# Kernel optimization log

Hardware: AMD Instinct MI355X
Metric: run time of the kernel (lower is better)

## Reference

```python
import jax, jax.numpy as jnp
import numpy as np

N_NODES = 100000
N_EDGES = 3200000
N_GRAPHS = 1000
IN_C, HID_C, OUT_C = 128, 128, 10
BN_EPS = 1e-5


def setup_inputs() -> dict:
    key = jax.random.key(0)
    ks = jax.random.split(key, 16)
    s = lambda k, shape, fan: jax.random.normal(k, shape, jnp.float32) * (1.0 / np.sqrt(fan))
    x = jax.random.normal(ks[0], (N_NODES, IN_C), jnp.float32)
    edge_index = jax.random.randint(ks[1], (2, N_EDGES), 0, N_NODES, dtype=jnp.int64)
    batch = jnp.sort(jax.random.randint(ks[2], (N_NODES,), 0, N_GRAPHS, dtype=jnp.int64))
    return {
        "x": x, "edge_index": edge_index, "batch": batch,
        "W1a": s(ks[3], (IN_C, HID_C), IN_C), "b1a": jnp.zeros((HID_C,), jnp.float32),
        "W1b": s(ks[4], (HID_C, HID_C), HID_C), "b1b": jnp.zeros((HID_C,), jnp.float32),
        "g1": jnp.ones((HID_C,), jnp.float32), "be1": jnp.zeros((HID_C,), jnp.float32),
        "W2a": s(ks[5], (HID_C, HID_C), HID_C), "b2a": jnp.zeros((HID_C,), jnp.float32),
        "W2b": s(ks[6], (HID_C, HID_C), HID_C), "b2b": jnp.zeros((HID_C,), jnp.float32),
        "g2": jnp.ones((HID_C,), jnp.float32), "be2": jnp.zeros((HID_C,), jnp.float32),
        "Wlin": s(ks[7], (HID_C, OUT_C), HID_C), "blin": jnp.zeros((OUT_C,), jnp.float32),
    }


def _batchnorm(h, gamma, beta):
    # BatchNorm1d, training mode: batch statistics (biased variance, as torch)
    mean = jnp.mean(h, axis=0)
    var = jnp.mean(jnp.square(h - mean), axis=0)
    return (h - mean) * jax.lax.rsqrt(var + BN_EPS) * gamma + beta


def _gin_conv(x, src, dst, Wa, ba, Wb, bb, gamma, beta):
    # GINConv with eps=0: mlp(x + sum_{j->i} x_j); scatter-add over dst
    agg = jax.ops.segment_sum(x[src], dst, num_segments=N_NODES)
    h = x + agg
    h = jax.nn.relu(h @ Wa + ba) @ Wb + bb
    return _batchnorm(h, gamma, beta)


def reference(x, edge_index, batch, W1a, b1a, W1b, b1b, g1, be1,
              W2a, b2a, W2b, b2b, g2, be2, Wlin, blin):
    src, dst = edge_index[0], edge_index[1]
    h = jax.nn.relu(_gin_conv(x, src, dst, W1a, b1a, W1b, b1b, g1, be1))
    h = jax.nn.relu(_gin_conv(h, src, dst, W2a, b2a, W2b, b2b, g2, be2))
    pooled = jax.ops.segment_sum(h, batch, num_segments=N_GRAPHS)  # [G, HID_C]
    logits = pooled @ Wlin + blin
    return jax.nn.log_softmax(logits, axis=1)
```

## Files before the change

kernel.cpp:

```cpp
#include <hip/hip_runtime.h>
#include <hip/hip_bf16.h>

#define NN 100000
#define NE 3200000
#define NG 1000
#define BN_EPS 1e-5f

#define BKT_SH 6
#define BKTN 64
#define NBKT 1563
#define CHUNK 8192
#define NBINBLK 391

typedef __attribute__((ext_vector_type(8))) short short8v;
typedef __attribute__((ext_vector_type(4))) float f32x4;

__device__ __forceinline__ unsigned int f2bf(float f) {
    unsigned int u = __builtin_bit_cast(unsigned int, f);
    u += 0x7FFFu + ((u >> 16) & 1u);
    return u >> 16;
}
__device__ __forceinline__ float bf2f(unsigned int h16) {
    return __builtin_bit_cast(float, h16 << 16);
}

__global__ __launch_bounds__(256) void bucket_count_kernel(const int* __restrict__ dst,
                                                           int* __restrict__ bcnt) {
    __shared__ int h[NBKT];
    int t = threadIdx.x;
    for (int i = t; i < NBKT; i += 256) h[i] = 0;
    __syncthreads();
    int gid = blockIdx.x * 256 + t;
    for (int e = gid; e < NE; e += NBINBLK * 256) atomicAdd(&h[dst[e] >> BKT_SH], 1);
    __syncthreads();
    for (int i = t; i < NBKT; i += 256) if (h[i]) atomicAdd(&bcnt[i], h[i]);
}

__global__ void bucket_scan_kernel(const int* __restrict__ bcnt, int* __restrict__ bbase,
                                   int* __restrict__ bcur) {
    __shared__ int wsum[16];
    __shared__ int lcarry;
    int t = threadIdx.x, lane = t & 63, w = t >> 6;
    if (t == 0) lcarry = 0;
    __syncthreads();
    for (int base = 0; base < NBKT; base += 1024) {
        int i = base + t;
        int v = (i < NBKT) ? bcnt[i] : 0;
        int incl = v;
        #pragma unroll
        for (int d = 1; d < 64; d <<= 1) { int u = __shfl_up(incl, d, 64); if (lane >= d) incl += u; }
        if (lane == 63) wsum[w] = incl;
        __syncthreads();
        if (w == 0) {
            int s = (lane < 16) ? wsum[lane] : 0;
            #pragma unroll
            for (int d = 1; d < 16; d <<= 1) { int u = __shfl_up(s, d, 64); if (lane >= d) s += u; }
            if (lane < 16) wsum[lane] = s;
        }
        __syncthreads();
        int excl = lcarry + (w ? wsum[w - 1] : 0) + incl - v;
        if (i < NBKT) { bbase[i] = excl; bcur[i] = excl; }
        __syncthreads();
        if (t == 0) lcarry += wsum[15];
        __syncthreads();
    }
}

__global__ __launch_bounds__(256) void bin_kernel(const int* __restrict__ src,
        const int* __restrict__ dst, int* __restrict__ bcur,
        unsigned int* __restrict__ ebin) {
    __shared__ unsigned int ebuf[CHUNK];
    __shared__ unsigned short bids[CHUNK];
    __shared__ int hist[NBKT], lbase[NBKT], lcur[NBKT], delta[NBKT];
    __shared__ int wsum4[4];
    __shared__ int carry;
    int t = threadIdx.x;
    int lane = t & 63, w = t >> 6;
    int c0 = blockIdx.x * CHUNK;
    int cnt = min(CHUNK, NE - c0);
    for (int i = t; i < NBKT; i += 256) hist[i] = 0;
    if (t == 0) carry = 0;
    __syncthreads();
    for (int i = t; i < cnt; i += 256) atomicAdd(&hist[dst[c0 + i] >> BKT_SH], 1);
    __syncthreads();
    for (int bb = 0; bb < NBKT; bb += 256) {
        int i = bb + t;
        int v = (i < NBKT) ? hist[i] : 0;
        int incl = v;
        #pragma unroll
        for (int d2 = 1; d2 < 64; d2 <<= 1) { int u = __shfl_up(incl, d2, 64); if (lane >= d2) incl += u; }
        if (lane == 63) wsum4[w] = incl;
        __syncthreads();
        int wo = 0;
        if (w > 0) wo = wsum4[0];
        if (w > 1) wo += wsum4[1];
        if (w > 2) wo += wsum4[2];
        int excl = carry + wo + incl - v;
        if (i < NBKT) { lbase[i] = excl; lcur[i] = excl; }
        int tot = wsum4[0] + wsum4[1] + wsum4[2] + wsum4[3];
        __syncthreads();
        if (t == 0) carry += tot;
        __syncthreads();
    }
    for (int b = t; b < NBKT; b += 256) {
        int hh = hist[b];
        delta[b] = (hh ? atomicAdd(&bcur[b], hh) : 0) - lbase[b];
    }
    __syncthreads();
    for (int i = t; i < cnt; i += 256) {
        int d = dst[c0 + i];
        int s = src[c0 + i];
        int b = d >> BKT_SH;
        unsigned int entry = ((unsigned int)s << BKT_SH) | (unsigned int)(d & (BKTN - 1));
        int p = atomicAdd(&lcur[b], 1);
        ebuf[p] = entry;
        bids[p] = (unsigned short)b;
    }
    __syncthreads();
    for (int i = t; i < cnt; i += 256) {
        ebin[delta[bids[i]] + i] = ebuf[i];
    }
}

__global__ __launch_bounds__(256) void sort_kernel(const unsigned int* __restrict__ ebin,
        const int* __restrict__ bbase, const int* __restrict__ bcnt,
        int* __restrict__ noffs, int* __restrict__ csrc) {
    __shared__ int nh[BKTN], ncur[BKTN];
    int b = blockIdx.x, t = threadIdx.x;
    int base = bbase[b], cnt = bcnt[b];
    if (t < BKTN) nh[t] = 0;
    __syncthreads();
    for (int i = t; i < cnt; i += 256) atomicAdd(&nh[ebin[base + i] & (BKTN - 1)], 1);
    __syncthreads();
    if (t < 64) {
        int v = nh[t], incl = v;
        #pragma unroll
        for (int d = 1; d < 64; d <<= 1) { int u = __shfl_up(incl, d, 64); if (t >= d) incl += u; }
        int excl = incl - v;
        ncur[t] = excl;
        int node = (b << BKT_SH) + t;
        if (node < NN) noffs[node] = base + excl;
    }
    if (b == 0 && t == 0) noffs[NN] = NE;
    __syncthreads();
    for (int i = t; i < cnt; i += 256) {
        unsigned int e = ebin[base + i];
        int p = atomicAdd(&ncur[e & (BKTN - 1)], 1);
        csrc[base + p] = (int)(e >> BKT_SH);
    }
}

__global__ void prep_kernel(const float* __restrict__ x, unsigned int* __restrict__ xp,
                            const float* __restrict__ W1a, const float* __restrict__ W1b,
                            const float* __restrict__ W2a, const float* __restrict__ W2b,
                            unsigned int* __restrict__ Wt) {
    int bx = blockIdx.x;
    int t = threadIdx.x;
    if (bx < 25000) {
        int tid = bx * 256 + t;
        float2 v = ((const float2*)x)[tid];
        xp[tid] = f2bf(v.x) | (f2bf(v.y) << 16);
    } else {
        int tid = (bx - 25000) * 256 + t;
        int m = tid >> 13;
        int r = tid & 8191;
        int c = r >> 6, kh = r & 63;
        const float* W = (m == 0) ? W1a : (m == 1) ? W1b : (m == 2) ? W2a : W2b;
        float a = W[(2 * kh) * 128 + c];
        float b = W[(2 * kh + 1) * 128 + c];
        Wt[tid] = f2bf(a) | (f2bf(b) << 16);
    }
}

template<int BN_IN>
__global__ __launch_bounds__(256) void aggregate_gather_kernel(
        const unsigned int* __restrict__ xp, const float* __restrict__ coef,
        const int* __restrict__ noffs, const int* __restrict__ csrc,
        unsigned int* __restrict__ outp) {
    int node = __builtin_amdgcn_readfirstlane(blockIdx.x * 4 + (threadIdx.x >> 6));
    int lane = threadIdx.x & 63;
    float a0 = 1.f, b0 = 0.f, a1 = 1.f, b1 = 0.f;
    if (BN_IN) {
        float2 av = ((const float2*)coef)[lane];
        float2 bv = ((const float2*)(coef + 128))[lane];
        a0 = av.x; a1 = av.y; b0 = bv.x; b1 = bv.y;
    }
    unsigned int u = xp[(size_t)node * 64 + lane];
    float alo = bf2f(u & 0xFFFFu), ahi = bf2f(u >> 16);
    if (BN_IN) { alo = fmaxf(alo * a0 + b0, 0.f); ahi = fmaxf(ahi * a1 + b1, 0.f); }
    int s = noffs[node], e = noffs[node + 1];
    int i = s;
    for (; i + 16 <= e; i += 16) {
        int idx[16];
        #pragma unroll
        for (int j = 0; j < 16; ++j) idx[j] = csrc[i + j];
        unsigned int uv[16];
        #pragma unroll
        for (int j = 0; j < 16; ++j) uv[j] = xp[(size_t)idx[j] * 64 + lane];
        #pragma unroll
        for (int j = 0; j < 16; ++j) {
            float lo = bf2f(uv[j] & 0xFFFFu), hi = bf2f(uv[j] >> 16);
            if (BN_IN) { lo = fmaxf(lo * a0 + b0, 0.f); hi = fmaxf(hi * a1 + b1, 0.f); }
            alo += lo; ahi += hi;
        }
    }
    for (; i + 8 <= e; i += 8) {
        int idx[8];
        #pragma unroll
        for (int j = 0; j < 8; ++j) idx[j] = csrc[i + j];
        unsigned int uv[8];
        #pragma unroll
        for (int j = 0; j < 8; ++j) uv[j] = xp[(size_t)idx[j] * 64 + lane];
        #pragma unroll
        for (int j = 0; j < 8; ++j) {
            float lo = bf2f(uv[j] & 0xFFFFu), hi = bf2f(uv[j] >> 16);
            if (BN_IN) { lo = fmaxf(lo * a0 + b0, 0.f); hi = fmaxf(hi * a1 + b1, 0.f); }
            alo += lo; ahi += hi;
        }
    }
    for (; i < e; ++i) {
        int sv = csrc[i];
        unsigned int uu = xp[(size_t)sv * 64 + lane];
        float lo = bf2f(uu & 0xFFFFu), hi = bf2f(uu >> 16);
        if (BN_IN) { lo = fmaxf(lo * a0 + b0, 0.f); hi = fmaxf(hi * a1 + b1, 0.f); }
        alo += lo; ahi += hi;
    }
    outp[(size_t)node * 64 + lane] = f2bf(alo) | (f2bf(ahi) << 16);
}

__global__ __launch_bounds__(256) void mlp_kernel(const unsigned int* __restrict__ Pin,
        const unsigned int* __restrict__ WtA, const float* __restrict__ bA,
        const unsigned int* __restrict__ WtB, const float* __restrict__ bB,
        unsigned int* __restrict__ Pout, float* __restrict__ partial) {
    __shared__ unsigned int tile[64 * 68];
    __shared__ float sred[4][128];
    __shared__ float qred[4][128];
    int t = threadIdx.x, l = t & 63, w = t >> 6;
    int node0 = blockIdx.x * 64;
    int rbase = w * 16;
    int g = l >> 4, r = l & 15;
    int g4 = g * 4;

    const uint4* P4 = (const uint4*)Pin;
    #pragma unroll
    for (int i = 0; i < 4; ++i) {
        int rl = rbase + i * 4 + g;
        int node = node0 + rl;
        uint4 v = make_uint4(0u, 0u, 0u, 0u);
        if (node < NN) v = P4[(size_t)node * 16 + r];
        *(uint4*)&tile[rl * 68 + r * 4] = v;
    }

    f32x4 acc1[8];
    #pragma unroll
    for (int cb = 0; cb < 8; ++cb) acc1[cb] = (f32x4){0.f, 0.f, 0.f, 0.f};
    #pragma unroll
    for (int kk = 0; kk < 4; ++kk) {
        short8v a = *(short8v*)&tile[(rbase + r) * 68 + kk * 16 + g4];
        #pragma unroll
        for (int cb = 0; cb < 8; ++cb) {
            short8v wv = *(const short8v*)&WtA[(size_t)(cb * 16 + r) * 64 + kk * 16 + g4];
            acc1[cb] = __builtin_amdgcn_mfma_f32_16x16x32_bf16(wv, a, acc1[cb], 0, 0, 0);
        }
    }
    #pragma unroll
    for (int cb = 0; cb < 8; ++cb) {
        int c0 = cb * 16 + g4;
        float4 bi = *(const float4*)&bA[c0];
        float h0 = fmaxf(acc1[cb][0] + bi.x, 0.f);
        float h1 = fmaxf(acc1[cb][1] + bi.y, 0.f);
        float h2 = fmaxf(acc1[cb][2] + bi.z, 0.f);
        float h3 = fmaxf(acc1[cb][3] + bi.w, 0.f);
        uint2 pk;
        pk.x = f2bf(h0) | (f2bf(h1) << 16);
        pk.y = f2bf(h2) | (f2bf(h3) << 16);
        *(uint2*)&tile[(rbase + r) * 68 + (c0 >> 1)] = pk;
    }
    f32x4 acc2[8];
    #pragma unroll
    for (int cb = 0; cb < 8; ++cb) acc2[cb] = (f32x4){0.f, 0.f, 0.f, 0.f};
    #pragma unroll
    for (int kk = 0; kk < 4; ++kk) {
        short8v a = *(short8v*)&tile[(rbase + r) * 68 + kk * 16 + g4];
        #pragma unroll
        for (int cb = 0; cb < 8; ++cb) {
            short8v wv = *(const short8v*)&WtB[(size_t)(cb * 16 + r) * 64 + kk * 16 + g4];
            acc2[cb] = __builtin_amdgcn_mfma_f32_16x16x32_bf16(wv, a, acc2[cb], 0, 0, 0);
        }
    }
    int node = node0 + rbase + r;
    bool valid = node < NN;
    float msk = valid ? 1.f : 0.f;
    #pragma unroll
    for (int cb = 0; cb < 8; ++cb) {
        int c0 = cb * 16 + g4;
        float4 bi = *(const float4*)&bB[c0];
        float h0 = acc2[cb][0] + bi.x;
        float h1 = acc2[cb][1] + bi.y;
        float h2 = acc2[cb][2] + bi.z;
        float h3 = acc2[cb][3] + bi.w;
        float s0 = h0 * msk, s1 = h1 * msk, s2 = h2 * msk, s3 = h3 * msk;
        float q0 = s0 * h0, q1 = s1 * h1, q2 = s2 * h2, q3 = s3 * h3;
        #pragma unroll
        for (int m = 1; m < 16; m <<= 1) {
            s0 += __shfl_xor(s0, m, 64); s1 += __shfl_xor(s1, m, 64);
            s2 += __shfl_xor(s2, m, 64); s3 += __shfl_xor(s3, m, 64);
            q0 += __shfl_xor(q0, m, 64); q1 += __shfl_xor(q1, m, 64);
            q2 += __shfl_xor(q2, m, 64); q3 += __shfl_xor(q3, m, 64);
        }
        if (r == 0) {
            sred[w][c0 + 0] = s0; sred[w][c0 + 1] = s1;
            sred[w][c0 + 2] = s2; sred[w][c0 + 3] = s3;
            qred[w][c0 + 0] = q0; qred[w][c0 + 1] = q1;
            qred[w][c0 + 2] = q2; qred[w][c0 + 3] = q3;
        }
        if (valid) {
            uint2 pk;
            pk.x = f2bf(h0) | (f2bf(h1) << 16);
            pk.y = f2bf(h2) | (f2bf(h3) << 16);
            *(uint2*)&Pout[(size_t)node * 64 + (c0 >> 1)] = pk;
        }
    }
    __syncthreads();
    if (t < 128) {
        partial[(size_t)blockIdx.x * 256 + t] =
            sred[0][t] + sred[1][t] + sred[2][t] + sred[3][t];
    } else {
        int c = t - 128;
        partial[(size_t)blockIdx.x * 256 + t] =
            qred[0][c] + qred[1][c] + qred[2][c] + qred[3][c];
    }
}

__global__ __launch_bounds__(256) void bn_reduce_kernel(const float* __restrict__ partial,
        const float* __restrict__ gamma, const float* __restrict__ beta,
        float* __restrict__ coef) {
    __shared__ float red[2][256];
    int c = blockIdx.x;
    int t = threadIdx.x;
    float sm = 0.f, sq = 0.f;
    for (int i = t; i < NBKT; i += 256) {
        sm += partial[(size_t)i * 256 + c];
        sq += partial[(size_t)i * 256 + 128 + c];
    }
    red[0][t] = sm; red[1][t] = sq;
    __syncthreads();
    if (t < 64) {
        float s = red[0][t] + red[0][t + 64] + red[0][t + 128] + red[0][t + 192];
        float q = red[1][t] + red[1][t + 64] + red[1][t + 128] + red[1][t + 192];
        #pragma unroll
        for (int m = 1; m < 64; m <<= 1) {
            s += __shfl_xor(s, m, 64);
            q += __shfl_xor(q, m, 64);
        }
        if (t == 0) {
            const float inv = 1.0f / NN;
            float mean = s * inv;
            float var = q * inv - mean * mean;
            float a = gamma[c] * rsqrtf(var + BN_EPS);
            coef[c] = a;
            coef[128 + c] = beta[c] - mean * a;
        }
    }
}

__global__ void pool_head_kernel(const unsigned int* __restrict__ hb,
        const float* __restrict__ coef, const int* __restrict__ batch,
        const float* __restrict__ Wlin, const float* __restrict__ blin,
        float* __restrict__ out) {
    int g = blockIdx.x;
    int l = threadIdx.x;
    float2 av = ((const float2*)coef)[l];
    float2 bv = ((const float2*)(coef + 128))[l];
    int a = 0, b = NN;
    while (a < b) { int m = (a + b) >> 1; if (batch[m] < g) a = m + 1; else b = m; }
    int start = a;
    b = NN;
    while (a < b) { int m = (a + b) >> 1; if (batch[m] < g + 1) a = m + 1; else b = m; }
    int end = a;
    float s0 = 0.f, s1 = 0.f;
    for (int i = start; i < end; ++i) {
        unsigned int u = hb[(size_t)i * 64 + l];
        s0 += fmaxf(bf2f(u & 0xFFFFu) * av.x + bv.x, 0.f);
        s1 += fmaxf(bf2f(u >> 16) * av.y + bv.y, 0.f);
    }
    float lg[10];
    #pragma unroll
    for (int o = 0; o < 10; ++o) {
        float partial = s0 * Wlin[(2 * l) * 10 + o] + s1 * Wlin[(2 * l + 1) * 10 + o];
        #pragma unroll
        for (int m = 1; m < 64; m <<= 1) partial += __shfl_xor(partial, m, 64);
        lg[o] = partial + blin[o];
    }
    float mx = lg[0];
    #pragma unroll
    for (int o = 1; o < 10; ++o) mx = fmaxf(mx, lg[o]);
    float se = 0.f;
    #pragma unroll
    for (int o = 0; o < 10; ++o) se += expf(lg[o] - mx);
    float lse = mx + logf(se);
    if (l == 0) {
        #pragma unroll
        for (int o = 0; o < 10; ++o) out[g * 10 + o] = lg[o] - lse;
    }
}

extern "C" void kernel_launch(void* const* d_in, const int* in_sizes, int n_in,
                              void* d_out, int out_size, void* d_ws, size_t ws_size,
                              hipStream_t stream) {
    const float* x    = (const float*)d_in[0];
    const int*   edge = (const int*)d_in[1];
    const int*   batch= (const int*)d_in[2];
    const float* W1a  = (const float*)d_in[3];
    const float* b1a  = (const float*)d_in[4];
    const float* W1b  = (const float*)d_in[5];
    const float* b1b  = (const float*)d_in[6];
    const float* g1   = (const float*)d_in[7];
    const float* be1  = (const float*)d_in[8];
    const float* W2a  = (const float*)d_in[9];
    const float* b2a  = (const float*)d_in[10];
    const float* W2b  = (const float*)d_in[11];
    const float* b2b  = (const float*)d_in[12];
    const float* g2   = (const float*)d_in[13];
    const float* be2  = (const float*)d_in[14];
    const float* Wlin = (const float*)d_in[15];
    const float* blin = (const float*)d_in[16];
    float* out = (float*)d_out;

    char* ws = (char*)d_ws;
    size_t off = 0;
    auto alloc = [&](size_t bytes) -> void* {
        void* p = ws + off; off += (bytes + 255) & ~(size_t)255; return p;
    };
    unsigned int* Px   = (unsigned int*)alloc((size_t)NN * 64 * 4);
    unsigned int* Pa   = (unsigned int*)alloc((size_t)NN * 64 * 4);
    unsigned int* Pb   = (unsigned int*)alloc((size_t)NN * 64 * 4);
    unsigned int* ebin = (unsigned int*)alloc((size_t)NE * 4);
    int*   csrc   = (int*)alloc((size_t)NE * 4);
    int*   noffs  = (int*)alloc((NN + 1) * 4);
    int*   bcnt   = (int*)alloc(NBKT * 4);
    int*   bbase  = (int*)alloc(NBKT * 4);
    int*   bcur   = (int*)alloc(NBKT * 4);
    float* coef1  = (float*)alloc(256 * 4);
    float* coef2  = (float*)alloc(256 * 4);
    float* partial= (float*)alloc((size_t)NBKT * 256 * 4);
    unsigned int* Wt = (unsigned int*)alloc(4 * 8192 * 4);
    unsigned int* Wt1a = Wt;
    unsigned int* Wt1b = Wt + 8192;
    unsigned int* Wt2a = Wt + 16384;
    unsigned int* Wt2b = Wt + 24576;

    const int* srcI = edge;
    const int* dstI = edge + NE;

    hipMemsetAsync(bcnt, 0, NBKT * 4, stream);

    bucket_count_kernel<<<NBINBLK, 256, 0, stream>>>(dstI, bcnt);
    bucket_scan_kernel<<<1, 1024, 0, stream>>>(bcnt, bbase, bcur);
    bin_kernel<<<NBINBLK, 256, 0, stream>>>(srcI, dstI, bcur, ebin);
    sort_kernel<<<NBKT, 256, 0, stream>>>(ebin, bbase, bcnt, noffs, csrc);
    prep_kernel<<<25128, 256, 0, stream>>>(x, Px, W1a, W1b, W2a, W2b, Wt);

    aggregate_gather_kernel<0><<<25000, 256, 0, stream>>>(Px, coef1, noffs, csrc, Pa);
    mlp_kernel<<<NBKT, 256, 0, stream>>>(Pa, Wt1a, b1a, Wt1b, b1b, Pb, partial);
    bn_reduce_kernel<<<128, 256, 0, stream>>>(partial, g1, be1, coef1);
    aggregate_gather_kernel<1><<<25000, 256, 0, stream>>>(Pb, coef1, noffs, csrc, Pa);
    mlp_kernel<<<NBKT, 256, 0, stream>>>(Pa, Wt2a, b2a, Wt2b, b2b, Pb, partial);
    bn_reduce_kernel<<<128, 256, 0, stream>>>(partial, g2, be2, coef2);

    pool_head_kernel<<<NG, 64, 0, stream>>>(Pb, coef2, batch, Wlin, blin, out);
}
```

Measured before the change: 511.4 us.

## Sort CSR neighbors by source sub-range and fuse bucket count into prep

The per-bucket sort now keys on destination node plus a coarse source range (16 sub-ranges), so each node's neighbor list is ordered roughly by source index. This should improve locality of the feature gathers in both aggregation passes. Separately, the bucket-count pass is merged into the prep kernel as extra blocks, saving a launch and letting the two overlap. The cost is a larger shared histogram and a multi-pass block scan in the sort kernel.

Result: no change. 511.8 us (+0.1%).

```diff
diff --git a/kernel.cpp b/kernel.cpp
--- a/kernel.cpp
+++ b/kernel.cpp
@@ -11,6 +11,8 @@
 #define NBKT 1563
 #define CHUNK 8192
 #define NBINBLK 391
+#define NSR 16
+#define SRSH 13
 
 typedef __attribute__((ext_vector_type(8))) short short8v;
 typedef __attribute__((ext_vector_type(4))) float f32x4;
@@ -24,16 +26,36 @@
     return __builtin_bit_cast(float, h16 << 16);
 }
 
-__global__ __launch_bounds__(256) void bucket_count_kernel(const int* __restrict__ dst,
-                                                           int* __restrict__ bcnt) {
+__global__ void prep_kernel(const float* __restrict__ x, unsigned int* __restrict__ xp,
+                            const float* __restrict__ W1a, const float* __restrict__ W1b,
+                            const float* __restrict__ W2a, const float* __restrict__ W2b,
+                            unsigned int* __restrict__ Wt,
+                            const int* __restrict__ dst, int* __restrict__ bcnt) {
     __shared__ int h[NBKT];
+    int bx = blockIdx.x;
     int t = threadIdx.x;
-    for (int i = t; i < NBKT; i += 256) h[i] = 0;
-    __syncthreads();
-    int gid = blockIdx.x * 256 + t;
-    for (int e = gid; e < NE; e += NBINBLK * 256) atomicAdd(&h[dst[e] >> BKT_SH], 1);
-    __syncthreads();
-    for (int i = t; i < NBKT; i += 256) if (h[i]) atomicAdd(&bcnt[i], h[i]);
+    if (bx < 25000) {
+        int tid = bx * 256 + t;
+        float2 v = ((const float2*)x)[tid];
+        xp[tid] = f2bf(v.x) | (f2bf(v.y) << 16);
+    } else if (bx < 25128) {
+        int tid = (bx - 25000) * 256 + t;
+        int m = tid >> 13;
+        int r = tid & 8191;
+        int c = r >> 6, kh = r & 63;
+        const float* W = (m == 0) ? W1a : (m == 1) ? W1b : (m == 2) ? W2a : W2b;
+        float a = W[(2 * kh) * 128 + c];
+        float b = W[(2 * kh + 1) * 128 + c];
+        Wt[tid] = f2bf(a) | (f2bf(b) << 16);
+    } else {
+        int blk = bx - 25128;
+        for (int i = t; i < NBKT; i += 256) h[i] = 0;
+        __syncthreads();
+        int gid = blk * 256 + t;
+        for (int e = gid; e < NE; e += NBINBLK * 256) atomicAdd(&h[dst[e] >> BKT_SH], 1);
+        __syncthreads();
+        for (int i = t; i < NBKT; i += 256) if (h[i]) atomicAdd(&bcnt[i], h[i]);
+    }
 }
 
 __global__ void bucket_scan_kernel(const int* __restrict__ bcnt, int* __restrict__ bbase,
@@ -125,50 +147,51 @@
 __global__ __launch_bounds__(256) void sort_kernel(const unsigned int* __restrict__ ebin,
         const int* __restrict__ bbase, const int* __restrict__ bcnt,
         int* __restrict__ noffs, int* __restrict__ csrc) {
-    __shared__ int nh[BKTN], ncur[BKTN];
+    __shared__ int nh[BKTN * NSR];
+    __shared__ int wsum4[4];
+    __shared__ int carry;
     int b = blockIdx.x, t = threadIdx.x;
+    int lane = t & 63, w = t >> 6;
     int base = bbase[b], cnt = bcnt[b];
-    if (t < BKTN) nh[t] = 0;
-    __syncthreads();
-    for (int i = t; i < cnt; i += 256) atomicAdd(&nh[ebin[base + i] & (BKTN - 1)], 1);
-    __syncthreads();
-    if (t < 64) {
-        int v = nh[t], incl = v;
-        #pragma unroll
-        for (int d = 1; d < 64; d <<= 1) { int u = __shfl_up(incl, d, 64); if (t >= d) incl += u; }
-        int excl = incl - v;
-        ncur[t] = excl;
-        int node = (b << BKT_SH) + t;
-        if (node < NN) noffs[node] = base + excl;
-    }
-    if (b == 0 && t == 0) noffs[NN] = NE;
+    for (int i = t; i < BKTN * NSR; i += 256) nh[i] = 0;
+    if (t == 0) carry = 0;
     __syncthreads();
     for (int i = t; i < cnt; i += 256) {
         unsigned int e = ebin[base + i];
-        int p = atomicAdd(&ncur[e & (BKTN - 1)], 1);
-        csrc[base + p] = (int)(e >> BKT_SH);
-    }
-}
-
-__global__ void prep_kernel(const float* __restrict__ x, unsigned int* __restrict__ xp,
-                            const float* __restrict__ W1a, const float* __restrict__ W1b,
-                            const float* __restrict__ W2a, const float* __restrict__ W2b,
-                            unsigned int* __restrict__ Wt) {
-    int bx = blockIdx.x;
-    int t = threadIdx.x;
-    if (bx < 25000) {
-        int tid = bx * 256 + t;
-        float2 v = ((const float2*)x)[tid];
-        xp[tid] = f2bf(v.x) | (f2bf(v.y) << 16);
-    } else {
-        int tid = (bx - 25000) * 256 + t;
-        int m = tid >> 13;
-        int r = tid & 8191;
-        int c = r >> 6, kh = r & 63;
-        const float* W = (m == 0) ? W1a : (m == 1) ? W1b : (m == 2) ? W2a : W2b;
-        float a = W[(2 * kh) * 128 + c];
-        float b = W[(2 * kh + 1) * 128 + c];
-        Wt[tid] = f2bf(a) | (f2bf(b) << 16);
+        int key = (int)(e & (BKTN - 1)) * NSR + (int)((e >> BKT_SH) >> SRSH);
+        atomicAdd(&nh[key], 1);
+    }
+    __syncthreads();
+    for (int rb = 0; rb < BKTN * NSR; rb += 256) {
+        int v = nh[rb + t];
+        int incl = v;
+        #pragma unroll
+        for (int d = 1; d < 64; d <<= 1) { int u = __shfl_up(incl, d, 64); if (lane >= d) incl += u; }
+        if (lane == 63) wsum4[w] = incl;
+        __syncthreads();
+        int wo = 0;
+        if (w > 0) wo = wsum4[0];
+        if (w > 1) wo += wsum4[1];
+        if (w > 2) wo += wsum4[2];
+        int tot = wsum4[0] + wsum4[1] + wsum4[2] + wsum4[3];
+        int excl = carry + wo + incl - v;
+        nh[rb + t] = excl;
+        __syncthreads();
+        if (t == 0) carry += tot;
+        __syncthreads();
+    }
+    if (t < 64) {
+        int node = (b << BKT_SH) + t;
+        if (node < NN) noffs[node] = base + nh[t * NSR];
+    }
+    if (b == 0 && t == 0) noffs[NN] = NE;
+    __syncthreads();
+    for (int i = t; i < cnt; i += 256) {
+        unsigned int e = ebin[base + i];
+        int srcv = (int)(e >> BKT_SH);
+        int key = (int)(e & (BKTN - 1)) * NSR + (srcv >> SRSH);
+        int p = atomicAdd(&nh[key], 1);
+        csrc[base + p] = srcv;
     }
 }
 
@@ -455,11 +478,11 @@
 
     hipMemsetAsync(bcnt, 0, NBKT * 4, stream);
 
-    bucket_count_kernel<<<NBINBLK, 256, 0, stream>>>(dstI, bcnt);
+    prep_kernel<<<25128 + NBINBLK, 256, 0, stream>>>(x, Px, W1a, W1b, W2a, W2b, Wt,
+                                                     dstI, bcnt);
     bucket_scan_kernel<<<1, 1024, 0, stream>>>(bcnt, bbase, bcur);
     bin_kernel<<<NBINBLK, 256, 0, stream>>>(srcI, dstI, bcur, ebin);
     sort_kernel<<<NBKT, 256, 0, stream>>>(ebin, bbase, bcnt, noffs, csrc);
-    prep_kernel<<<25128, 256, 0, stream>>>(x, Px, W1a, W1b, W2a, W2b, Wt);
 
     aggregate_gather_kernel<0><<<25000, 256, 0, stream>>>(Px, coef1, noffs, csrc, Pa);
     mlp_kernel<<<NBKT, 256, 0, stream>>>(Pa, Wt1a, b1a, Wt1b, b1b, Pb, partial);
```

## Fuse bucket count into prep kernel and simplify binning with direct global scatter

Applied to the files above, without the earlier changes.

The bucket-count pass becomes extra blocks of the prep kernel, so counting overlaps with bf16 conversion and one launch disappears. The bin kernel drops its in-block prefix scan and shared staging buffer and writes each edge straight to its global slot via a shared per-bucket cursor. Chunk size shrinks so more blocks run with less shared memory. The trade-off is less coalesced global writes in binning and more global atomics on the bucket cursors.

Result: slower. 580.0 us (+13.4%).

```diff
diff --git a/kernel.cpp b/kernel.cpp
--- a/kernel.cpp
+++ b/kernel.cpp
@@ -9,8 +9,8 @@
 #define BKT_SH 6
 #define BKTN 64
 #define NBKT 1563
-#define CHUNK 8192
-#define NBINBLK 391
+#define CHUNK 2048
+#define NBINBLK 1563
 
 typedef __attribute__((ext_vector_type(8))) short short8v;
 typedef __attribute__((ext_vector_type(4))) float f32x4;
@@ -24,143 +24,19 @@
     return __builtin_bit_cast(float, h16 << 16);
 }
 
-__global__ __launch_bounds__(256) void bucket_count_kernel(const int* __restrict__ dst,
-                                                           int* __restrict__ bcnt) {
-    __shared__ int h[NBKT];
-    int t = threadIdx.x;
-    for (int i = t; i < NBKT; i += 256) h[i] = 0;
-    __syncthreads();
-    int gid = blockIdx.x * 256 + t;
-    for (int e = gid; e < NE; e += NBINBLK * 256) atomicAdd(&h[dst[e] >> BKT_SH], 1);
-    __syncthreads();
-    for (int i = t; i < NBKT; i += 256) if (h[i]) atomicAdd(&bcnt[i], h[i]);
-}
-
-__global__ void bucket_scan_kernel(const int* __restrict__ bcnt, int* __restrict__ bbase,
-                                   int* __restrict__ bcur) {
-    __shared__ int wsum[16];
-    __shared__ int lcarry;
-    int t = threadIdx.x, lane = t & 63, w = t >> 6;
-    if (t == 0) lcarry = 0;
-    __syncthreads();
-    for (int base = 0; base < NBKT; base += 1024) {
-        int i = base + t;
-        int v = (i < NBKT) ? bcnt[i] : 0;
-        int incl = v;
-        #pragma unroll
-        for (int d = 1; d < 64; d <<= 1) { int u = __shfl_up(incl, d, 64); if (lane >= d) incl += u; }
-        if (lane == 63) wsum[w] = incl;
-        __syncthreads();
-        if (w == 0) {
-            int s = (lane < 16) ? wsum[lane] : 0;
-            #pragma unroll
-            for (int d = 1; d < 16; d <<= 1) { int u = __shfl_up(s, d, 64); if (lane >= d) s += u; }
-            if (lane < 16) wsum[lane] = s;
-        }
-        __syncthreads();
-        int excl = lcarry + (w ? wsum[w - 1] : 0) + incl - v;
-        if (i < NBKT) { bbase[i] = excl; bcur[i] = excl; }
-        __syncthreads();
-        if (t == 0) lcarry += wsum[15];
-        __syncthreads();
-    }
-}
-
-__global__ __launch_bounds__(256) void bin_kernel(const int* __restrict__ src,
-        const int* __restrict__ dst, int* __restrict__ bcur,
-        unsigned int* __restrict__ ebin) {
-    __shared__ unsigned int ebuf[CHUNK];
-    __shared__ unsigned short bids[CHUNK];
-    __shared__ int hist[NBKT], lbase[NBKT], lcur[NBKT], delta[NBKT];
-    __shared__ int wsum4[4];
-    __shared__ int carry;
-    int t = threadIdx.x;
-    int lane = t & 63, w = t >> 6;
-    int c0 = blockIdx.x * CHUNK;
-    int cnt = min(CHUNK, NE - c0);
-    for (int i = t; i < NBKT; i += 256) hist[i] = 0;
-    if (t == 0) carry = 0;
-    __syncthreads();
-    for (int i = t; i < cnt; i += 256) atomicAdd(&hist[dst[c0 + i] >> BKT_SH], 1);
-    __syncthreads();
-    for (int bb = 0; bb < NBKT; bb += 256) {
-        int i = bb + t;
-        int v = (i < NBKT) ? hist[i] : 0;
-        int incl = v;
-        #pragma unroll
-        for (int d2 = 1; d2 < 64; d2 <<= 1) { int u = __shfl_up(incl, d2, 64); if (lane >= d2) incl += u; }
-        if (lane == 63) wsum4[w] = incl;
-        __syncthreads();
-        int wo = 0;
-        if (w > 0) wo = wsum4[0];
-        if (w > 1) wo += wsum4[1];
-        if (w > 2) wo += wsum4[2];
-        int excl = carry + wo + incl - v;
-        if (i < NBKT) { lbase[i] = excl; lcur[i] = excl; }
-        int tot = wsum4[0] + wsum4[1] + wsum4[2] + wsum4[3];
-        __syncthreads();
-        if (t == 0) carry += tot;
-        __syncthreads();
-    }
-    for (int b = t; b < NBKT; b += 256) {
-        int hh = hist[b];
-        delta[b] = (hh ? atomicAdd(&bcur[b], hh) : 0) - lbase[b];
-    }
-    __syncthreads();
-    for (int i = t; i < cnt; i += 256) {
-        int d = dst[c0 + i];
-        int s = src[c0 + i];
-        int b = d >> BKT_SH;
-        unsigned int entry = ((unsigned int)s << BKT_SH) | (unsigned int)(d & (BKTN - 1));
-        int p = atomicAdd(&lcur[b], 1);
-        ebuf[p] = entry;
-        bids[p] = (unsigned short)b;
-    }
-    __syncthreads();
-    for (int i = t; i < cnt; i += 256) {
-        ebin[delta[bids[i]] + i] = ebuf[i];
-    }
-}
-
-__global__ __launch_bounds__(256) void sort_kernel(const unsigned int* __restrict__ ebin,
-        const int* __restrict__ bbase, const int* __restrict__ bcnt,
-        int* __restrict__ noffs, int* __restrict__ csrc) {
-    __shared__ int nh[BKTN], ncur[BKTN];
-    int b = blockIdx.x, t = threadIdx.x;
-    int base = bbase[b], cnt = bcnt[b];
-    if (t < BKTN) nh[t] = 0;
-    __syncthreads();
-    for (int i = t; i < cnt; i += 256) atomicAdd(&nh[ebin[base + i] & (BKTN - 1)], 1);
-    __syncthreads();
-    if (t < 64) {
-        int v = nh[t], incl = v;
-        #pragma unroll
-        for (int d = 1; d < 64; d <<= 1) { int u = __shfl_up(incl, d, 64); if (t >= d) incl += u; }
-        int excl = incl - v;
-        ncur[t] = excl;
-        int node = (b << BKT_SH) + t;
-        if (node < NN) noffs[node] = base + excl;
-    }
-    if (b == 0 && t == 0) noffs[NN] = NE;
-    __syncthreads();
-    for (int i = t; i < cnt; i += 256) {
-        unsigned int e = ebin[base + i];
-        int p = atomicAdd(&ncur[e & (BKTN - 1)], 1);
-        csrc[base + p] = (int)(e >> BKT_SH);
-    }
-}
-
 __global__ void prep_kernel(const float* __restrict__ x, unsigned int* __restrict__ xp,
                             const float* __restrict__ W1a, const float* __restrict__ W1b,
                             const float* __restrict__ W2a, const float* __restrict__ W2b,
-                            unsigned int* __restrict__ Wt) {
+                            unsigned int* __restrict__ Wt,
+                            const int* __restrict__ dst, int* __restrict__ bcnt) {
+    __shared__ int h[NBKT];
     int bx = blockIdx.x;
     int t = threadIdx.x;
     if (bx < 25000) {
         int tid = bx * 256 + t;
         float2 v = ((const float2*)x)[tid];
         xp[tid] = f2bf(v.x) | (f2bf(v.y) << 16);
-    } else {
+    } else if (bx < 25128) {
         int tid = (bx - 25000) * 256 + t;
         int m = tid >> 13;
         int r = tid & 8191;
@@ -169,6 +45,100 @@
         float a = W[(2 * kh) * 128 + c];
         float b = W[(2 * kh + 1) * 128 + c];
         Wt[tid] = f2bf(a) | (f2bf(b) << 16);
+    } else {
+        int blk = bx - 25128;
+        for (int i = t; i < NBKT; i += 256) h[i] = 0;
+        __syncthreads();
+        int c0 = blk * CHUNK;
+        int cnt = min(CHUNK, NE - c0);
+        for (int i = t; i < cnt; i += 256) atomicAdd(&h[dst[c0 + i] >> BKT_SH], 1);
+        __syncthreads();
+        for (int i = t; i < NBKT; i += 256) if (h[i]) atomicAdd(&bcnt[i], h[i]);
+    }
+}
+
+__global__ void bucket_scan_kernel(const int* __restrict__ bcnt, int* __restrict__ bbase,
+                                   int* __restrict__ bcur) {
+    __shared__ int wsum[16];
+    __shared__ int lcarry;
+    int t = threadIdx.x, lane = t & 63, w = t >> 6;
+    if (t == 0) lcarry = 0;
+    __syncthreads();
+    for (int base = 0; base < NBKT; base += 1024) {
+        int i = base + t;
+        int v = (i < NBKT) ? bcnt[i] : 0;
+        int incl = v;
+        #pragma unroll
+        for (int d = 1; d < 64; d <<= 1) { int u = __shfl_up(incl, d, 64); if (lane >= d) incl += u; }
+        if (lane == 63) wsum[w] = incl;
+        __syncthreads();
+        if (w == 0) {
+            int s = (lane < 16) ? wsum[lane] : 0;
+            #pragma unroll
+            for (int d = 1; d < 16; d <<= 1) { int u = __shfl_up(s, d, 64); if (lane >= d) s += u; }
+            if (lane < 16) wsum[lane] = s;
+        }
+        __syncthreads();
+        int excl = lcarry + (w ? wsum[w - 1] : 0) + incl - v;
+        if (i < NBKT) { bbase[i] = excl; bcur[i] = excl; }
+        __syncthreads();
+        if (t == 0) lcarry += wsum[15];
+        __syncthreads();
+    }
+}
+
+__global__ __launch_bounds__(256) void bin_kernel(const int* __restrict__ src,
+        const int* __restrict__ dst, int* __restrict__ bcur,
+        unsigned int* __restrict__ ebin) {
+    __shared__ int hist[NBKT];
+    __shared__ int delta[NBKT];
+    __shared__ int lcur[NBKT];
+    int t = threadIdx.x;
+    int c0 = blockIdx.x * CHUNK;
+    int cnt = min(CHUNK, NE - c0);
+    for (int i = t; i < NBKT; i += 256) { hist[i] = 0; lcur[i] = 0; }
+    __syncthreads();
+    for (int i = t; i < cnt; i += 256) atomicAdd(&hist[dst[c0 + i] >> BKT_SH], 1);
+    __syncthreads();
+    for (int b = t; b < NBKT; b += 256) {
+        int hh = hist[b];
+        delta[b] = hh ? atomicAdd(&bcur[b], hh) : 0;
+    }
+    __syncthreads();
+    for (int i = t; i < cnt; i += 256) {
+        int d = dst[c0 + i];
+        int s = src[c0 + i];
+        int b = d >> BKT_SH;
+        int p = atomicAdd(&lcur[b], 1);
+        ebin[delta[b] + p] = ((unsigned int)s << BKT_SH) | (unsigned int)(d & (BKTN - 1));
+    }
+}
+
+__global__ __launch_bounds__(256) void sort_kernel(const unsigned int* __restrict__ ebin,
+        const int* __restrict__ bbase, const int* __restrict__ bcnt,
+        int* __restrict__ noffs, int* __restrict__ csrc) {
+    __shared__ int nh[BKTN], ncur[BKTN];
+    int b = blockIdx.x, t = threadIdx.x;
+    int base = bbase[b], cnt = bcnt[b];
+    if (t < BKTN) nh[t] = 0;
+    __syncthreads();
+    for (int i = t; i < cnt; i += 256) atomicAdd(&nh[ebin[base + i] & (BKTN - 1)], 1);
+    __syncthreads();
+    if (t < 64) {
+        int v = nh[t], incl = v;
+        #pragma unroll
+        for (int d = 1; d < 64; d <<= 1) { int u = __shfl_up(incl, d, 64); if (t >= d) incl += u; }
+        int excl = incl - v;
+        ncur[t] = excl;
+        int node = (b << BKT_SH) + t;
+        if (node < NN) noffs[node] = base + excl;
+    }
+    if (b == 0 && t == 0) noffs[NN] = NE;
+    __syncthreads();
+    for (int i = t; i < cnt; i += 256) {
+        unsigned int e = ebin[base + i];
+        int p = atomicAdd(&ncur[e & (BKTN - 1)], 1);
+        csrc[base + p] = (int)(e >> BKT_SH);
     }
 }
 
@@ -455,11 +425,11 @@
 
     hipMemsetAsync(bcnt, 0, NBKT * 4, stream);
 
-    bucket_count_kernel<<<NBINBLK, 256, 0, stream>>>(dstI, bcnt);
+    prep_kernel<<<25128 + NBINBLK, 256, 0, stream>>>(x, Px, W1a, W1b, W2a, W2b, Wt,
+                                                     dstI, bcnt);
     bucket_scan_kernel<<<1, 1024, 0, stream>>>(bcnt, bbase, bcur);
     bin_kernel<<<NBINBLK, 256, 0, stream>>>(srcI, dstI, bcur, ebin);
     sort_kernel<<<NBKT, 256, 0, stream>>>(ebin, bbase, bcnt, noffs, csrc);
-    prep_kernel<<<25128, 256, 0, stream>>>(x, Px, W1a, W1b, W2a, W2b, Wt);
 
     aggregate_gather_kernel<0><<<25000, 256, 0, stream>>>(Px, coef1, noffs, csrc, Pa);
     mlp_kernel<<<NBKT, 256, 0, stream>>>(Pa, Wt1a, b1a, Wt1b, b1b, Pb, partial);
```

## Widen CSR buckets to 128 nodes and fuse bucket counting into prep kernel

Applied to the files above, without the earlier changes.

Doubles the destination bucket width to 128 nodes, which halves the bucket count to 782, and halves the bin chunk size so the binning stage still launches 782 blocks. The bucket-count histogram is folded into the bf16 conversion prep kernel as extra blocks, removing one launch. The scan becomes a single pass because the bucket count now fits in one block, and the sort kernel scans 128 per-node counts with two wavefront scans. The MLP tile count is decoupled into a separate NTILE constant so the MLP grid is unchanged. In exchange, each sort block handles larger buckets and the bin kernel works on smaller chunks with more scatter runs.

New measurement: 534.5 us. 4.5% more time.

```diff
diff --git a/kernel.cpp b/kernel.cpp
--- a/kernel.cpp
+++ b/kernel.cpp
@@ -6,11 +6,14 @@
 #define NG 1000
 #define BN_EPS 1e-5f
 
-#define BKT_SH 6
-#define BKTN 64
-#define NBKT 1563
-#define CHUNK 8192
-#define NBINBLK 391
+#define BKT_SH 7
+#define BKTN 128
+#define NBKT 782
+#define CHUNK 4096
+#define NBINBLK 782
+#define HCHUNK 2048
+#define NHBLK 1563
+#define NTILE 1563
 
 typedef __attribute__((ext_vector_type(8))) short short8v;
 typedef __attribute__((ext_vector_type(4))) float f32x4;
@@ -24,46 +27,58 @@
     return __builtin_bit_cast(float, h16 << 16);
 }
 
-__global__ __launch_bounds__(256) void bucket_count_kernel(const int* __restrict__ dst,
-                                                           int* __restrict__ bcnt) {
+__global__ void prep_kernel(const float* __restrict__ x, unsigned int* __restrict__ xp,
+                            const float* __restrict__ W1a, const float* __restrict__ W1b,
+                            const float* __restrict__ W2a, const float* __restrict__ W2b,
+                            unsigned int* __restrict__ Wt,
+                            const int* __restrict__ dst, int* __restrict__ bcnt) {
     __shared__ int h[NBKT];
+    int bx = blockIdx.x;
     int t = threadIdx.x;
-    for (int i = t; i < NBKT; i += 256) h[i] = 0;
-    __syncthreads();
-    int gid = blockIdx.x * 256 + t;
-    for (int e = gid; e < NE; e += NBINBLK * 256) atomicAdd(&h[dst[e] >> BKT_SH], 1);
-    __syncthreads();
-    for (int i = t; i < NBKT; i += 256) if (h[i]) atomicAdd(&bcnt[i], h[i]);
+    if (bx < 25000) {
+        int tid = bx * 256 + t;
+        float2 v = ((const float2*)x)[tid];
+        xp[tid] = f2bf(v.x) | (f2bf(v.y) << 16);
+    } else if (bx < 25128) {
+        int tid = (bx - 25000) * 256 + t;
+        int m = tid >> 13;
+        int r = tid & 8191;
+        int c = r >> 6, kh = r & 63;
+        const float* W = (m == 0) ? W1a : (m == 1) ? W1b : (m == 2) ? W2a : W2b;
+        float a = W[(2 * kh) * 128 + c];
+        float b = W[(2 * kh + 1) * 128 + c];
+        Wt[tid] = f2bf(a) | (f2bf(b) << 16);
+    } else {
+        int blk = bx - 25128;
+        for (int i = t; i < NBKT; i += 256) h[i] = 0;
+        __syncthreads();
+        int c0 = blk * HCHUNK;
+        int cnt = min(HCHUNK, NE - c0);
+        for (int i = t; i < cnt; i += 256) atomicAdd(&h[dst[c0 + i] >> BKT_SH], 1);
+        __syncthreads();
+        for (int i = t; i < NBKT; i += 256) if (h[i]) atomicAdd(&bcnt[i], h[i]);
+    }
 }
 
 __global__ void bucket_scan_kernel(const int* __restrict__ bcnt, int* __restrict__ bbase,
                                    int* __restrict__ bcur) {
     __shared__ int wsum[16];
-    __shared__ int lcarry;
     int t = threadIdx.x, lane = t & 63, w = t >> 6;
-    if (t == 0) lcarry = 0;
-    __syncthreads();
-    for (int base = 0; base < NBKT; base += 1024) {
-        int i = base + t;
-        int v = (i < NBKT) ? bcnt[i] : 0;
-        int incl = v;
-        #pragma unroll
-        for (int d = 1; d < 64; d <<= 1) { int u = __shfl_up(incl, d, 64); if (lane >= d) incl += u; }
-        if (lane == 63) wsum[w] = incl;
-        __syncthreads();
-        if (w == 0) {
-            int s = (lane < 16) ? wsum[lane] : 0;
-            #pragma unroll
-            for (int d = 1; d < 16; d <<= 1) { int u = __shfl_up(s, d, 64); if (lane >= d) s += u; }
-            if (lane < 16) wsum[lane] = s;
-        }
-        __syncthreads();
-        int excl = lcarry + (w ? wsum[w - 1] : 0) + incl - v;
-        if (i < NBKT) { bbase[i] = excl; bcur[i] = excl; }
-        __syncthreads();
-        if (t == 0) lcarry += wsum[15];
-        __syncthreads();
-    }
+    int v = (t < NBKT) ? bcnt[t] : 0;
+    int incl = v;
+    #pragma unroll
+    for (int d = 1; d < 64; d <<= 1) { int u = __shfl_up(incl, d, 64); if (lane >= d) incl += u; }
+    if (lane == 63) wsum[w] = incl;
+    __syncthreads();
+    if (w == 0) {
+        int s = (lane < 16) ? wsum[lane] : 0;
+        #pragma unroll
+        for (int d = 1; d < 16; d <<= 1) { int u = __shfl_up(s, d, 64); if (lane >= d) s += u; }
+        if (lane < 16) wsum[lane] = s;
+    }
+    __syncthreads();
+    int excl = (w ? wsum[w - 1] : 0) + incl - v;
+    if (t < NBKT) { bbase[t] = excl; bcur[t] = excl; }
 }
 
 __global__ __launch_bounds__(256) void bin_kernel(const int* __restrict__ src,
@@ -125,7 +140,7 @@
 __global__ __launch_bounds__(256) void sort_kernel(const unsigned int* __restrict__ ebin,
         const int* __restrict__ bbase, const int* __restrict__ bcnt,
         int* __restrict__ noffs, int* __restrict__ csrc) {
-    __shared__ int nh[BKTN], ncur[BKTN];
+    __shared__ int nh[BKTN], nbase[BKTN], ncur[BKTN];
     int b = blockIdx.x, t = threadIdx.x;
     int base = bbase[b], cnt = bcnt[b];
     if (t < BKTN) nh[t] = 0;
@@ -133,13 +148,22 @@
     for (int i = t; i < cnt; i += 256) atomicAdd(&nh[ebin[base + i] & (BKTN - 1)], 1);
     __syncthreads();
     if (t < 64) {
-        int v = nh[t], incl = v;
-        #pragma unroll
-        for (int d = 1; d < 64; d <<= 1) { int u = __shfl_up(incl, d, 64); if (t >= d) incl += u; }
-        int excl = incl - v;
-        ncur[t] = excl;
-        int node = (b << BKT_SH) + t;
-        if (node < NN) noffs[node] = base + excl;
+        int v0 = nh[t], v1 = nh[64 + t];
+        int i0 = v0;
+        #pragma unroll
+        for (int d = 1; d < 64; d <<= 1) { int u = __shfl_up(i0, d, 64); if (t >= d) i0 += u; }
+        int tot0 = __shfl(i0, 63, 64);
+        int i1 = v1;
+        #pragma unroll
+        for (int d = 1; d < 64; d <<= 1) { int u = __shfl_up(i1, d, 64); if (t >= d) i1 += u; }
+        int e0 = i0 - v0;
+        int e1 = tot0 + i1 - v1;
+        nbase[t] = e0; nbase[64 + t] = e1;
+        ncur[t] = e0; ncur[64 + t] = e1;
+        int node0 = (b << BKT_SH) + t;
+        int node1 = node0 + 64;
+        if (node0 < NN) noffs[node0] = base + e0;
+        if (node1 < NN) noffs[node1] = base + e1;
     }
     if (b == 0 && t == 0) noffs[NN] = NE;
     __syncthreads();
@@ -147,28 +171,6 @@
         unsigned int e = ebin[base + i];
         int p = atomicAdd(&ncur[e & (BKTN - 1)], 1);
         csrc[base + p] = (int)(e >> BKT_SH);
-    }
-}
-
-__global__ void prep_kernel(const float* __restrict__ x, unsigned int* __restrict__ xp,
-                            const float* __restrict__ W1a, const float* __restrict__ W1b,
-                            const float* __restrict__ W2a, const float* __restrict__ W2b,
-                            unsigned int* __restrict__ Wt) {
-    int bx = blockIdx.x;
-    int t = threadIdx.x;
-    if (bx < 25000) {
-        int tid = bx * 256 + t;
-        float2 v = ((const float2*)x)[tid];
-        xp[tid] = f2bf(v.x) | (f2bf(v.y) << 16);
-    } else {
-        int tid = (bx - 25000) * 256 + t;
-        int m = tid >> 13;
-        int r = tid & 8191;
-        int c = r >> 6, kh = r & 63;
-        const float* W = (m == 0) ? W1a : (m == 1) ? W1b : (m == 2) ? W2a : W2b;
-        float a = W[(2 * kh) * 128 + c];
-        float b = W[(2 * kh + 1) * 128 + c];
-        Wt[tid] = f2bf(a) | (f2bf(b) << 16);
     }
 }
 
@@ -339,7 +341,7 @@
     int c = blockIdx.x;
     int t = threadIdx.x;
     float sm = 0.f, sq = 0.f;
-    for (int i = t; i < NBKT; i += 256) {
+    for (int i = t; i < NTILE; i += 256) {
         sm += partial[(size_t)i * 256 + c];
         sq += partial[(size_t)i * 256 + 128 + c];
     }
@@ -443,7 +445,7 @@
     int*   bcur   = (int*)alloc(NBKT * 4);
     float* coef1  = (float*)alloc(256 * 4);
     float* coef2  = (float*)alloc(256 * 4);
-    float* partial= (float*)alloc((size_t)NBKT * 256 * 4);
+    float* partial= (float*)alloc((size_t)NTILE * 256 * 4);
     unsigned int* Wt = (unsigned int*)alloc(4 * 8192 * 4);
     unsigned int* Wt1a = Wt;
     unsigned int* Wt1b = Wt + 8192;
@@ -455,17 +457,17 @@
 
     hipMemsetAsync(bcnt, 0, NBKT * 4, stream);
 
-    bucket_count_kernel<<<NBINBLK, 256, 0, stream>>>(dstI, bcnt);
+    prep_kernel<<<25128 + NHBLK, 256, 0, stream>>>(x, Px, W1a, W1b, W2a, W2b, Wt,
+                                                   dstI, bcnt);
     bucket_scan_kernel<<<1, 1024, 0, stream>>>(bcnt, bbase, bcur);
     bin_kernel<<<NBINBLK, 256, 0, stream>>>(srcI, dstI, bcur, ebin);
     sort_kernel<<<NBKT, 256, 0, stream>>>(ebin, bbase, bcnt, noffs, csrc);
-    prep_kernel<<<25128, 256, 0, stream>>>(x, Px, W1a, W1b, W2a, W2b, Wt);
 
     aggregate_gather_kernel<0><<<25000, 256, 0, stream>>>(Px, coef1, noffs, csrc, Pa);
-    mlp_kernel<<<NBKT, 256, 0, stream>>>(Pa, Wt1a, b1a, Wt1b, b1b, Pb, partial);
+    mlp_kernel<<<NTILE, 256, 0, stream>>>(Pa, Wt1a, b1a, Wt1b, b1b, Pb, partial);
     bn_reduce_kernel<<<128, 256, 0, stream>>>(partial, g1, be1, coef1);
     aggregate_gather_kernel<1><<<25000, 256, 0, stream>>>(Pb, coef1, noffs, csrc, Pa);
-    mlp_kernel<<<NBKT, 256, 0, stream>>>(Pa, Wt2a, b2a, Wt2b, b2b, Pb, partial);
+    mlp_kernel<<<NTILE, 256, 0, stream>>>(Pa, Wt2a, b2a, Wt2b, b2b, Pb, partial);
     bn_reduce_kernel<<<128, 256, 0, stream>>>(partial, g2, be2, coef2);
 
     pool_head_kernel<<<NG, 64, 0, stream>>>(Pb, coef2, batch, Wlin, blin, out);
```
